# Kernel optimization log

Measured on AMD Instinct MI355X. Metric: run time of the kernel, lower is better.

The kernel has to match this reference:

```python
import jax, jax.numpy as jnp
import numpy as np

N = 1024
DIM = 128
HEADS = 8
DK = DIM // HEADS
EDIM = 16
EPS = 1e-5
NEG = -10000.0


def _lin(k, din, dout):
    return jax.random.normal(k, (din, dout), jnp.float32) * (1.0 / np.sqrt(din))


def setup_inputs() -> dict:
    key = jax.random.key(0)
    ks = jax.random.split(key, 10)
    mask = jax.random.randint(ks[2], (N, N), 0, 2).astype(bool)
    mask = mask | jnp.eye(N, dtype=bool)  # self-loops always valid
    return {
        "x": jax.random.normal(ks[0], (N, DIM), jnp.float32),
        "edge_feat": jax.random.normal(ks[1], (N, N, EDIM), jnp.float32),
        "mask": mask,
        "Wq": _lin(ks[3], DIM, DIM), "bq": jnp.zeros((DIM,), jnp.float32),
        "Wk": _lin(ks[4], DIM, DIM), "bk": jnp.zeros((DIM,), jnp.float32),
        "Wv": _lin(ks[5], DIM, DIM), "bv": jnp.zeros((DIM,), jnp.float32),
        "Wae": _lin(ks[6], EDIM, HEADS), "bae": jnp.zeros((HEADS,), jnp.float32),
        "Wve": _lin(ks[7], EDIM, DIM), "bve": jnp.zeros((DIM,), jnp.float32),
        "Wo": _lin(ks[8], DIM, DIM), "bo": jnp.zeros((DIM,), jnp.float32),
        "gamma": jnp.ones((DIM,), jnp.float32),
        "beta": jnp.zeros((DIM,), jnp.float32),
    }


def reference(x, edge_feat, mask, Wq, bq, Wk, bk, Wv, bv, Wae, bae, Wve, bve, Wo, bo, gamma, beta):
    n, dim = x.shape
    heads = bae.shape[0]
    dk = dim // heads
    # pre-LayerNorm
    mu = jnp.mean(x, axis=-1, keepdims=True)
    var = jnp.mean(jnp.square(x - mu), axis=-1, keepdims=True)
    h = (x - mu) * jax.lax.rsqrt(var + EPS) * gamma + beta
    q = (h @ Wq + bq).reshape(n, heads, dk)
    k = (h @ Wk + bk).reshape(n, heads, dk)
    v = (h @ Wv + bv).reshape(n, heads, dk)
    # attention logits with per-edge additive bias: (n, m, heads)
    att = jnp.einsum('nhd,mhd->nmh', q, k) / np.sqrt(dk).astype(np.float32)
    att = att + edge_feat @ Wae + bae
    att = jnp.where(mask[..., None], att, NEG)
    alpha = jax.nn.softmax(att, axis=1)  # softmax over source nodes m
    # edge-conditioned values: msg_{nm} = v_m + U(e_{nm})
    edge_val = (edge_feat @ Wve + bve).reshape(n, n, heads, dk)
    out = jnp.einsum('nmh,mhd->nhd', alpha, v) + jnp.einsum('nmh,nmhd->nhd', alpha, edge_val)
    out = out.reshape(n, dim) @ Wo + bo
    return x + out
```

## Files before the change

### kernel.cpp

```cpp
#include <hip/hip_runtime.h>
#include <hip/hip_bf16.h>

#define NNODE 1024
#define DIM 128
#define HEADS 8
#define DK 16
#define EDIM 16
#define BN 8
#define MR 32
#define KV_ROW 160
#define H_STRIDE 20
#define EF_ROW 20
#define EF_NSTR 644
#define LOG2E 1.44269504f

__global__ __launch_bounds__(384)
void ln_qkv_kernel(const float* __restrict__ x,
                   const float* __restrict__ Wq, const float* __restrict__ bq,
                   const float* __restrict__ Wk, const float* __restrict__ bk,
                   const float* __restrict__ Wv, const float* __restrict__ bv,
                   const float* __restrict__ gamma, const float* __restrict__ beta,
                   float* __restrict__ qg, float* __restrict__ kg, float* __restrict__ vg) {
    const int n = blockIdx.x;
    const int t = threadIdx.x;
    __shared__ float hrow[DIM];
    __shared__ float part[4];

    float xv = 0.f;
    if (t < 128) {
        xv = x[n * DIM + t];
        float v = xv;
        #pragma unroll
        for (int off = 32; off >= 1; off >>= 1) v += __shfl_xor(v, off);
        if ((t & 63) == 0) part[t >> 6] = v;
    }
    __syncthreads();
    const float mu = (part[0] + part[1]) * (1.0f / DIM);
    const float dx = xv - mu;
    if (t < 128) {
        float v = dx * dx;
        #pragma unroll
        for (int off = 32; off >= 1; off >>= 1) v += __shfl_xor(v, off);
        if ((t & 63) == 0) part[2 + (t >> 6)] = v;
    }
    __syncthreads();
    if (t < 128) {
        const float var = (part[2] + part[3]) * (1.0f / DIM);
        hrow[t] = dx * rsqrtf(var + 1e-5f) * gamma[t] + beta[t];
    }
    __syncthreads();

    const int which = t >> 7;
    const int col = t & 127;
    const float* W = (which == 0) ? Wq : (which == 1) ? Wk : Wv;
    const float* b = (which == 0) ? bq : (which == 1) ? bk : bv;
    float* o       = (which == 0) ? qg : (which == 1) ? kg : vg;
    float acc = b[col];
    #pragma unroll 16
    for (int i = 0; i < DIM; ++i) acc = fmaf(hrow[i], W[i * DIM + col], acc);
    o[n * DIM + col] = acc;
}

__global__ __launch_bounds__(256, 2)
void attn_kernel(const float* __restrict__ qg, const float* __restrict__ kg,
                 const float* __restrict__ vg, const float* __restrict__ ef,
                 const int* __restrict__ mask,
                 const float* __restrict__ Wae, const float* __restrict__ bae,
                 float* __restrict__ acc) {
    const int t = threadIdx.x;
    const int s  = t >> 5;
    const int np = (t >> 3) & 3;
    const int h  = t & 7;
    const int wid = t >> 6, lane = t & 63;
    const int bx = blockIdx.x;
    const int n0 = (bx >> 5) * BN;
    const int mb = (bx & 31) * MR;

    __shared__ float ef_lds[BN * EF_NSTR];
    __shared__ float kv_buf[2 * MR * KV_ROW];
    __shared__ int   mk_lds[BN * 34];

    float* k_lds = kv_buf;
    float* v_lds = kv_buf + MR * KV_ROW;

    #pragma unroll
    for (int r = 0; r < 4; ++r) {
        const int idx = t + 256 * r;
        const int nn = idx >> 7;
        const int mm = (idx >> 2) & 31;
        const int q4 = idx & 3;
        const float4 ev = *(const float4*)(ef + ((size_t)(n0 + nn) * NNODE + mb + mm) * EDIM + q4 * 4);
        *(float4*)&ef_lds[nn * EF_NSTR + mm * EF_ROW + q4 * 4] = ev;
    }
    #pragma unroll
    for (int r = 0; r < 4; ++r) {
        const int idx = t + 256 * r;
        const int mm = idx >> 5, c4 = idx & 31;
        const int hh = c4 >> 2, d4 = c4 & 3;
        const float4 kq = *(const float4*)(kg + (size_t)(mb + mm) * DIM + c4 * 4);
        const float4 vq = *(const float4*)(vg + (size_t)(mb + mm) * DIM + c4 * 4);
        *(float4*)&k_lds[mm * KV_ROW + hh * H_STRIDE + d4 * 4] = kq;
        *(float4*)&v_lds[mm * KV_ROW + hh * H_STRIDE + d4 * 4] = vq;
    }
    {
        const int nn = t >> 5, mm = t & 31;
        mk_lds[nn * 34 + mm] = mask[(size_t)(n0 + nn) * NNODE + (mb + mm)];
    }
    float qreg[2][DK];
    #pragma unroll
    for (int hf = 0; hf < 2; ++hf) {
        const float* qp = qg + (size_t)(n0 + np + 4 * hf) * DIM + h * DK;
        #pragma unroll
        for (int d4 = 0; d4 < 4; ++d4) {
            const float4 qv = *(const float4*)(qp + d4 * 4);
            qreg[hf][d4 * 4 + 0] = qv.x; qreg[hf][d4 * 4 + 1] = qv.y;
            qreg[hf][d4 * 4 + 2] = qv.z; qreg[hf][d4 * 4 + 3] = qv.w;
        }
    }
    float waec[EDIM];
    #pragma unroll
    for (int e = 0; e < EDIM; ++e) waec[e] = Wae[e * HEADS + h] * LOG2E;
    const float baeh = bae[h] * LOG2E;

    float sl[2] = {0.f, 0.f};
    float accv[2][DK], accT[2][EDIM];
    #pragma unroll
    for (int hf = 0; hf < 2; ++hf) {
        #pragma unroll
        for (int d = 0; d < DK; ++d) accv[hf][d] = 0.f;
        #pragma unroll
        for (int e = 0; e < EDIM; ++e) accT[hf][e] = 0.f;
    }

    __syncthreads();

    #pragma unroll
    for (int j = 0; j < 4; ++j) {
        const int m = j * 8 + s;
        float kk[DK], vv[DK];
        const float* kp = &k_lds[m * KV_ROW + h * H_STRIDE];
        const float* vp = &v_lds[m * KV_ROW + h * H_STRIDE];
        #pragma unroll
        for (int d4 = 0; d4 < 4; ++d4) {
            const float4 k4 = *(const float4*)(kp + d4 * 4);
            kk[d4 * 4 + 0] = k4.x; kk[d4 * 4 + 1] = k4.y;
            kk[d4 * 4 + 2] = k4.z; kk[d4 * 4 + 3] = k4.w;
            const float4 v4 = *(const float4*)(vp + d4 * 4);
            vv[d4 * 4 + 0] = v4.x; vv[d4 * 4 + 1] = v4.y;
            vv[d4 * 4 + 2] = v4.z; vv[d4 * 4 + 3] = v4.w;
        }
        #pragma unroll
        for (int hf = 0; hf < 2; ++hf) {
            const int n = np + 4 * hf;
            const float* ep = &ef_lds[n * EF_NSTR + m * EF_ROW];
            float efv[EDIM];
            #pragma unroll
            for (int e4 = 0; e4 < 4; ++e4) {
                const float4 ev = *(const float4*)(ep + e4 * 4);
                efv[e4 * 4 + 0] = ev.x; efv[e4 * 4 + 1] = ev.y;
                efv[e4 * 4 + 2] = ev.z; efv[e4 * 4 + 3] = ev.w;
            }
            float bias = baeh, dot = 0.f;
            #pragma unroll
            for (int e = 0; e < EDIM; ++e) bias = fmaf(efv[e], waec[e], bias);
            #pragma unroll
            for (int d = 0; d < DK; ++d) dot = fmaf(qreg[hf][d], kk[d], dot);
            const float lg = fmaf(dot, 0.25f * LOG2E, bias);
            const float p = mk_lds[n * 34 + m] ? __builtin_amdgcn_exp2f(lg) : 0.f;
            sl[hf] += p;
            #pragma unroll
            for (int d = 0; d < DK; ++d) accv[hf][d] = fmaf(p, vv[d], accv[hf][d]);
            #pragma unroll
            for (int e = 0; e < EDIM; ++e) accT[hf][e] = fmaf(p, efv[e], accT[hf][e]);
        }
    }

    #pragma unroll
    for (int hf = 0; hf < 2; ++hf) {
        sl[hf] += __shfl_xor(sl[hf], 32);
        #pragma unroll
        for (int d = 0; d < DK; ++d) accv[hf][d] += __shfl_xor(accv[hf][d], 32);
        #pragma unroll
        for (int e = 0; e < EDIM; ++e) accT[hf][e] += __shfl_xor(accT[hf][e], 32);
    }
    __syncthreads();
    float* red = kv_buf;
    if (lane < 32) {
        float* rp = &red[((wid * 4 + np) * 8 + h) * 66];
        #pragma unroll
        for (int hf = 0; hf < 2; ++hf) {
            rp[hf * 33 + 0] = sl[hf];
            #pragma unroll
            for (int d = 0; d < DK; ++d) rp[hf * 33 + 1 + d] = accv[hf][d];
            #pragma unroll
            for (int e = 0; e < EDIM; ++e) rp[hf * 33 + 17 + e] = accT[hf][e];
        }
    }
    __syncthreads();
    for (int v = t; v < BN * HEADS * 33; v += 256) {
        const int n = v / 264;
        const int rem = v - n * 264;
        const int hh = rem / 33;
        const int idx = rem - hh * 33;
        const int nnp = n & 3, hf = n >> 2;
        float sum = 0.f;
        #pragma unroll
        for (int w = 0; w < 4; ++w)
            sum += red[((w * 4 + nnp) * 8 + hh) * 66 + hf * 33 + idx];
        atomicAdd(&acc[((size_t)(n0 + n) * HEADS + hh) * 33 + idx], sum);
    }
}

__global__ __launch_bounds__(128)
void final_kernel(const float* __restrict__ acc,
                  const float* __restrict__ Wve, const float* __restrict__ bve,
                  const float* __restrict__ x,
                  const float* __restrict__ Wo, const float* __restrict__ bo,
                  float* __restrict__ out) {
    const int n = blockIdx.x, t = threadIdx.x;
    __shared__ float ab[HEADS * 33];
    __shared__ float orow[DIM];
    for (int u = t; u < HEADS * 33; u += 128) ab[u] = acc[(size_t)n * HEADS * 33 + u];
    __syncthreads();
    const int col = t, hh = col >> 4, dd = col & 15;
    const float slv = ab[hh * 33];
    float acc2 = 0.f;
    #pragma unroll
    for (int e = 0; e < EDIM; ++e) acc2 = fmaf(ab[hh * 33 + 17 + e], Wve[e * DIM + col], acc2);
    orow[col] = (ab[hh * 33 + 1 + dd] + acc2) / slv + bve[col];
    __syncthreads();
    float o = bo[col] + x[(size_t)n * DIM + col];
    #pragma unroll 16
    for (int i = 0; i < DIM; ++i) o = fmaf(orow[i], Wo[i * DIM + col], o);
    out[(size_t)n * DIM + col] = o;
}

extern "C" void kernel_launch(void* const* d_in, const int* in_sizes, int n_in,
                              void* d_out, int out_size, void* d_ws, size_t ws_size,
                              hipStream_t stream) {
    const float* x     = (const float*)d_in[0];
    const float* ef    = (const float*)d_in[1];
    const int*   mask  = (const int*)d_in[2];
    const float* Wq    = (const float*)d_in[3];
    const float* bq    = (const float*)d_in[4];
    const float* Wk    = (const float*)d_in[5];
    const float* bk    = (const float*)d_in[6];
    const float* Wv    = (const float*)d_in[7];
    const float* bv    = (const float*)d_in[8];
    const float* Wae   = (const float*)d_in[9];
    const float* bae   = (const float*)d_in[10];
    const float* Wve   = (const float*)d_in[11];
    const float* bve   = (const float*)d_in[12];
    const float* Wo    = (const float*)d_in[13];
    const float* bo    = (const float*)d_in[14];
    const float* gamma = (const float*)d_in[15];
    const float* beta  = (const float*)d_in[16];

    float* ws = (float*)d_ws;
    float* accb = ws;
    float* qg   = ws + 270336;
    float* kg   = qg + (size_t)NNODE * DIM;
    float* vg   = kg + (size_t)NNODE * DIM;

    hipMemsetAsync(accb, 0, (size_t)NNODE * HEADS * 33 * sizeof(float), stream);
    ln_qkv_kernel<<<NNODE, 384, 0, stream>>>(x, Wq, bq, Wk, bk, Wv, bv, gamma, beta, qg, kg, vg);
    attn_kernel<<<(NNODE / BN) * 32, 256, 0, stream>>>(qg, kg, vg, ef, mask, Wae, bae, accb);
    final_kernel<<<NNODE, 128, 0, stream>>>(accb, Wve, bve, x, Wo, bo, (float*)d_out);
}
```

Before: 183.3 us.

## Stage attention tiles in two smaller LDS chunks to raise occupancy

The attention kernel now loads the 32-source tile in two 16-source chunks, which shrinks LDS for edge features, K/V and mask. The launch bound moves from 2 to 4 blocks per SM. The cross-wave reduction becomes LDS atomics into a zeroed buffer in place of the write-then-sum pass, followed by a flat global atomic add. This trades one extra barrier and serialized per-chunk loads, plus LDS atomic contention, for higher occupancy and less shared memory.

```diff
diff --git a/kernel.cpp b/kernel.cpp
--- a/kernel.cpp
+++ b/kernel.cpp
@@ -8,10 +8,11 @@
 #define EDIM 16
 #define BN 8
 #define MR 32
+#define MC 16
 #define KV_ROW 160
 #define H_STRIDE 20
 #define EF_ROW 20
-#define EF_NSTR 644
+#define EF_NSTR 324
 #define LOG2E 1.44269504f
 
 __global__ __launch_bounds__(384)
@@ -61,7 +62,7 @@
     o[n * DIM + col] = acc;
 }
 
-__global__ __launch_bounds__(256, 2)
+__global__ __launch_bounds__(256, 4)
 void attn_kernel(const float* __restrict__ qg, const float* __restrict__ kg,
                  const float* __restrict__ vg, const float* __restrict__ ef,
                  const int* __restrict__ mask,
@@ -71,41 +72,19 @@
     const int s  = t >> 5;
     const int np = (t >> 3) & 3;
     const int h  = t & 7;
-    const int wid = t >> 6, lane = t & 63;
+    const int lane = t & 63;
     const int bx = blockIdx.x;
     const int n0 = (bx >> 5) * BN;
     const int mb = (bx & 31) * MR;
 
     __shared__ float ef_lds[BN * EF_NSTR];
-    __shared__ float kv_buf[2 * MR * KV_ROW];
-    __shared__ int   mk_lds[BN * 34];
-
-    float* k_lds = kv_buf;
-    float* v_lds = kv_buf + MR * KV_ROW;
-
-    #pragma unroll
-    for (int r = 0; r < 4; ++r) {
-        const int idx = t + 256 * r;
-        const int nn = idx >> 7;
-        const int mm = (idx >> 2) & 31;
-        const int q4 = idx & 3;
-        const float4 ev = *(const float4*)(ef + ((size_t)(n0 + nn) * NNODE + mb + mm) * EDIM + q4 * 4);
-        *(float4*)&ef_lds[nn * EF_NSTR + mm * EF_ROW + q4 * 4] = ev;
-    }
-    #pragma unroll
-    for (int r = 0; r < 4; ++r) {
-        const int idx = t + 256 * r;
-        const int mm = idx >> 5, c4 = idx & 31;
-        const int hh = c4 >> 2, d4 = c4 & 3;
-        const float4 kq = *(const float4*)(kg + (size_t)(mb + mm) * DIM + c4 * 4);
-        const float4 vq = *(const float4*)(vg + (size_t)(mb + mm) * DIM + c4 * 4);
-        *(float4*)&k_lds[mm * KV_ROW + hh * H_STRIDE + d4 * 4] = kq;
-        *(float4*)&v_lds[mm * KV_ROW + hh * H_STRIDE + d4 * 4] = vq;
-    }
-    {
-        const int nn = t >> 5, mm = t & 31;
-        mk_lds[nn * 34 + mm] = mask[(size_t)(n0 + nn) * NNODE + (mb + mm)];
-    }
+    __shared__ float k_lds[MC * KV_ROW];
+    __shared__ float v_lds[MC * KV_ROW];
+    __shared__ float red[BN * HEADS * 33];
+    __shared__ int   mk_lds[BN * 18];
+
+    for (int u = t; u < BN * HEADS * 33; u += 256) red[u] = 0.f;
+
     float qreg[2][DK];
     #pragma unroll
     for (int hf = 0; hf < 2; ++hf) {
@@ -132,46 +111,75 @@
         for (int e = 0; e < EDIM; ++e) accT[hf][e] = 0.f;
     }
 
-    __syncthreads();
-
-    #pragma unroll
-    for (int j = 0; j < 4; ++j) {
-        const int m = j * 8 + s;
-        float kk[DK], vv[DK];
-        const float* kp = &k_lds[m * KV_ROW + h * H_STRIDE];
-        const float* vp = &v_lds[m * KV_ROW + h * H_STRIDE];
-        #pragma unroll
-        for (int d4 = 0; d4 < 4; ++d4) {
-            const float4 k4 = *(const float4*)(kp + d4 * 4);
-            kk[d4 * 4 + 0] = k4.x; kk[d4 * 4 + 1] = k4.y;
-            kk[d4 * 4 + 2] = k4.z; kk[d4 * 4 + 3] = k4.w;
-            const float4 v4 = *(const float4*)(vp + d4 * 4);
-            vv[d4 * 4 + 0] = v4.x; vv[d4 * 4 + 1] = v4.y;
-            vv[d4 * 4 + 2] = v4.z; vv[d4 * 4 + 3] = v4.w;
-        }
-        #pragma unroll
-        for (int hf = 0; hf < 2; ++hf) {
-            const int n = np + 4 * hf;
-            const float* ep = &ef_lds[n * EF_NSTR + m * EF_ROW];
-            float efv[EDIM];
-            #pragma unroll
-            for (int e4 = 0; e4 < 4; ++e4) {
-                const float4 ev = *(const float4*)(ep + e4 * 4);
-                efv[e4 * 4 + 0] = ev.x; efv[e4 * 4 + 1] = ev.y;
-                efv[e4 * 4 + 2] = ev.z; efv[e4 * 4 + 3] = ev.w;
+    #pragma unroll
+    for (int c = 0; c < 2; ++c) {
+        const int mcb = mb + c * MC;
+        if (c) __syncthreads();
+
+        #pragma unroll
+        for (int r = 0; r < 2; ++r) {
+            const int idx = t + 256 * r;
+            const int nn = idx >> 6;
+            const int mm = (idx >> 2) & 15;
+            const int q4 = idx & 3;
+            const float4 ev = *(const float4*)(ef + ((size_t)(n0 + nn) * NNODE + mcb + mm) * EDIM + q4 * 4);
+            *(float4*)&ef_lds[nn * EF_NSTR + mm * EF_ROW + q4 * 4] = ev;
+        }
+        #pragma unroll
+        for (int r = 0; r < 2; ++r) {
+            const int idx = t + 256 * r;
+            const int mm = idx >> 5, c4 = idx & 31;
+            const int hh = c4 >> 2, d4 = c4 & 3;
+            const float4 kq = *(const float4*)(kg + (size_t)(mcb + mm) * DIM + c4 * 4);
+            const float4 vq = *(const float4*)(vg + (size_t)(mcb + mm) * DIM + c4 * 4);
+            *(float4*)&k_lds[mm * KV_ROW + hh * H_STRIDE + d4 * 4] = kq;
+            *(float4*)&v_lds[mm * KV_ROW + hh * H_STRIDE + d4 * 4] = vq;
+        }
+        if (t < BN * MC) {
+            const int nn = t >> 4, mm = t & 15;
+            mk_lds[nn * 18 + mm] = mask[(size_t)(n0 + nn) * NNODE + mcb + mm];
+        }
+        __syncthreads();
+
+        #pragma unroll
+        for (int j = 0; j < 2; ++j) {
+            const int m = j * 8 + s;
+            float kk[DK], vv[DK];
+            const float* kp = &k_lds[m * KV_ROW + h * H_STRIDE];
+            const float* vp = &v_lds[m * KV_ROW + h * H_STRIDE];
+            #pragma unroll
+            for (int d4 = 0; d4 < 4; ++d4) {
+                const float4 k4 = *(const float4*)(kp + d4 * 4);
+                kk[d4 * 4 + 0] = k4.x; kk[d4 * 4 + 1] = k4.y;
+                kk[d4 * 4 + 2] = k4.z; kk[d4 * 4 + 3] = k4.w;
+                const float4 v4 = *(const float4*)(vp + d4 * 4);
+                vv[d4 * 4 + 0] = v4.x; vv[d4 * 4 + 1] = v4.y;
+                vv[d4 * 4 + 2] = v4.z; vv[d4 * 4 + 3] = v4.w;
             }
-            float bias = baeh, dot = 0.f;
-            #pragma unroll
-            for (int e = 0; e < EDIM; ++e) bias = fmaf(efv[e], waec[e], bias);
-            #pragma unroll
-            for (int d = 0; d < DK; ++d) dot = fmaf(qreg[hf][d], kk[d], dot);
-            const float lg = fmaf(dot, 0.25f * LOG2E, bias);
-            const float p = mk_lds[n * 34 + m] ? __builtin_amdgcn_exp2f(lg) : 0.f;
-            sl[hf] += p;
-            #pragma unroll
-            for (int d = 0; d < DK; ++d) accv[hf][d] = fmaf(p, vv[d], accv[hf][d]);
-            #pragma unroll
-            for (int e = 0; e < EDIM; ++e) accT[hf][e] = fmaf(p, efv[e], accT[hf][e]);
+            #pragma unroll
+            for (int hf = 0; hf < 2; ++hf) {
+                const int n = np + 4 * hf;
+                const float* ep = &ef_lds[n * EF_NSTR + m * EF_ROW];
+                float efv[EDIM];
+                #pragma unroll
+                for (int e4 = 0; e4 < 4; ++e4) {
+                    const float4 ev = *(const float4*)(ep + e4 * 4);
+                    efv[e4 * 4 + 0] = ev.x; efv[e4 * 4 + 1] = ev.y;
+                    efv[e4 * 4 + 2] = ev.z; efv[e4 * 4 + 3] = ev.w;
+                }
+                float bias = baeh, dot = 0.f;
+                #pragma unroll
+                for (int e = 0; e < EDIM; ++e) bias = fmaf(efv[e], waec[e], bias);
+                #pragma unroll
+                for (int d = 0; d < DK; ++d) dot = fmaf(qreg[hf][d], kk[d], dot);
+                const float lg = fmaf(dot, 0.25f * LOG2E, bias);
+                const float p = mk_lds[n * 18 + m] ? __builtin_amdgcn_exp2f(lg) : 0.f;
+                sl[hf] += p;
+                #pragma unroll
+                for (int d = 0; d < DK; ++d) accv[hf][d] = fmaf(p, vv[d], accv[hf][d]);
+                #pragma unroll
+                for (int e = 0; e < EDIM; ++e) accT[hf][e] = fmaf(p, efv[e], accT[hf][e]);
+            }
         }
     }
 
@@ -183,32 +191,20 @@
         #pragma unroll
         for (int e = 0; e < EDIM; ++e) accT[hf][e] += __shfl_xor(accT[hf][e], 32);
     }
-    __syncthreads();
-    float* red = kv_buf;
     if (lane < 32) {
-        float* rp = &red[((wid * 4 + np) * 8 + h) * 66];
         #pragma unroll
         for (int hf = 0; hf < 2; ++hf) {
-            rp[hf * 33 + 0] = sl[hf];
-            #pragma unroll
-            for (int d = 0; d < DK; ++d) rp[hf * 33 + 1 + d] = accv[hf][d];
-            #pragma unroll
-            for (int e = 0; e < EDIM; ++e) rp[hf * 33 + 17 + e] = accT[hf][e];
-        }
-    }
-    __syncthreads();
-    for (int v = t; v < BN * HEADS * 33; v += 256) {
-        const int n = v / 264;
-        const int rem = v - n * 264;
-        const int hh = rem / 33;
-        const int idx = rem - hh * 33;
-        const int nnp = n & 3, hf = n >> 2;
-        float sum = 0.f;
-        #pragma unroll
-        for (int w = 0; w < 4; ++w)
-            sum += red[((w * 4 + nnp) * 8 + hh) * 66 + hf * 33 + idx];
-        atomicAdd(&acc[((size_t)(n0 + n) * HEADS + hh) * 33 + idx], sum);
-    }
+            float* rp = &red[((np + 4 * hf) * 8 + h) * 33];
+            atomicAdd(&rp[0], sl[hf]);
+            #pragma unroll
+            for (int d = 0; d < DK; ++d) atomicAdd(&rp[1 + d], accv[hf][d]);
+            #pragma unroll
+            for (int e = 0; e < EDIM; ++e) atomicAdd(&rp[17 + e], accT[hf][e]);
+        }
+    }
+    __syncthreads();
+    for (int u = t; u < BN * HEADS * 33; u += 256)
+        atomicAdd(&acc[(size_t)n0 * HEADS * 33 + u], red[u]);
 }
 
 __global__ __launch_bounds__(128)
```

Result: slower. 527.6 us (+187.8%).

## Read K/V directly from global memory and reuse edge-feature LDS for reduction

Applied to the files above, without the earlier changes.

Drops the shared-memory staging of K and V tiles. The attention loop now loads them straight from global memory through the cache, and that loop is no longer unrolled. The cross-wave reduction is rebuilt to reuse the edge-feature LDS buffer as two partial-sum arrays, with waves 2–3 accumulating into the values written by waves 0–1. The aim is to cut LDS footprint (raising occupancy) and staging overhead, at the cost of more global/L2 loads per thread, less instruction-level parallelism from the un-unrolled loop, and an extra barrier stage.

```diff
diff --git a/kernel.cpp b/kernel.cpp
--- a/kernel.cpp
+++ b/kernel.cpp
@@ -8,8 +8,6 @@
 #define EDIM 16
 #define BN 8
 #define MR 32
-#define KV_ROW 160
-#define H_STRIDE 20
 #define EF_ROW 20
 #define EF_NSTR 644
 #define LOG2E 1.44269504f
@@ -77,11 +75,7 @@
     const int mb = (bx & 31) * MR;
 
     __shared__ float ef_lds[BN * EF_NSTR];
-    __shared__ float kv_buf[2 * MR * KV_ROW];
     __shared__ int   mk_lds[BN * 34];
-
-    float* k_lds = kv_buf;
-    float* v_lds = kv_buf + MR * KV_ROW;
 
     #pragma unroll
     for (int r = 0; r < 4; ++r) {
@@ -92,16 +86,6 @@
         const float4 ev = *(const float4*)(ef + ((size_t)(n0 + nn) * NNODE + mb + mm) * EDIM + q4 * 4);
         *(float4*)&ef_lds[nn * EF_NSTR + mm * EF_ROW + q4 * 4] = ev;
     }
-    #pragma unroll
-    for (int r = 0; r < 4; ++r) {
-        const int idx = t + 256 * r;
-        const int mm = idx >> 5, c4 = idx & 31;
-        const int hh = c4 >> 2, d4 = c4 & 3;
-        const float4 kq = *(const float4*)(kg + (size_t)(mb + mm) * DIM + c4 * 4);
-        const float4 vq = *(const float4*)(vg + (size_t)(mb + mm) * DIM + c4 * 4);
-        *(float4*)&k_lds[mm * KV_ROW + hh * H_STRIDE + d4 * 4] = kq;
-        *(float4*)&v_lds[mm * KV_ROW + hh * H_STRIDE + d4 * 4] = vq;
-    }
     {
         const int nn = t >> 5, mm = t & 31;
         mk_lds[nn * 34 + mm] = mask[(size_t)(n0 + nn) * NNODE + (mb + mm)];
@@ -134,12 +118,13 @@
 
     __syncthreads();
 
-    #pragma unroll
+    #pragma unroll 1
     for (int j = 0; j < 4; ++j) {
         const int m = j * 8 + s;
+        const size_t gm = (size_t)(mb + m);
         float kk[DK], vv[DK];
-        const float* kp = &k_lds[m * KV_ROW + h * H_STRIDE];
-        const float* vp = &v_lds[m * KV_ROW + h * H_STRIDE];
+        const float* kp = kg + gm * DIM + h * DK;
+        const float* vp = vg + gm * DIM + h * DK;
         #pragma unroll
         for (int d4 = 0; d4 < 4; ++d4) {
             const float4 k4 = *(const float4*)(kp + d4 * 4);
@@ -184,31 +169,36 @@
         for (int e = 0; e < EDIM; ++e) accT[hf][e] += __shfl_xor(accT[hf][e], 32);
     }
     __syncthreads();
-    float* red = kv_buf;
-    if (lane < 32) {
-        float* rp = &red[((wid * 4 + np) * 8 + h) * 66];
+    float* redA = ef_lds;
+    float* redB = ef_lds + BN * HEADS * 33;
+    if (lane < 32 && wid < 2) {
+        float* base = (wid == 0) ? redA : redB;
         #pragma unroll
         for (int hf = 0; hf < 2; ++hf) {
-            rp[hf * 33 + 0] = sl[hf];
-            #pragma unroll
-            for (int d = 0; d < DK; ++d) rp[hf * 33 + 1 + d] = accv[hf][d];
-            #pragma unroll
-            for (int e = 0; e < EDIM; ++e) rp[hf * 33 + 17 + e] = accT[hf][e];
-        }
-    }
-    __syncthreads();
-    for (int v = t; v < BN * HEADS * 33; v += 256) {
-        const int n = v / 264;
-        const int rem = v - n * 264;
-        const int hh = rem / 33;
-        const int idx = rem - hh * 33;
-        const int nnp = n & 3, hf = n >> 2;
-        float sum = 0.f;
-        #pragma unroll
-        for (int w = 0; w < 4; ++w)
-            sum += red[((w * 4 + nnp) * 8 + hh) * 66 + hf * 33 + idx];
-        atomicAdd(&acc[((size_t)(n0 + n) * HEADS + hh) * 33 + idx], sum);
-    }
+            float* rp = base + ((np + 4 * hf) * 8 + h) * 33;
+            rp[0] = sl[hf];
+            #pragma unroll
+            for (int d = 0; d < DK; ++d) rp[1 + d] = accv[hf][d];
+            #pragma unroll
+            for (int e = 0; e < EDIM; ++e) rp[17 + e] = accT[hf][e];
+        }
+    }
+    __syncthreads();
+    if (lane < 32 && wid >= 2) {
+        float* base = (wid == 2) ? redA : redB;
+        #pragma unroll
+        for (int hf = 0; hf < 2; ++hf) {
+            float* rp = base + ((np + 4 * hf) * 8 + h) * 33;
+            rp[0] += sl[hf];
+            #pragma unroll
+            for (int d = 0; d < DK; ++d) rp[1 + d] += accv[hf][d];
+            #pragma unroll
+            for (int e = 0; e < EDIM; ++e) rp[17 + e] += accT[hf][e];
+        }
+    }
+    __syncthreads();
+    for (int u = t; u < BN * HEADS * 33; u += 256)
+        atomicAdd(&acc[(size_t)n0 * HEADS * 33 + u], redA[u] + redB[u]);
 }
 
 __global__ __launch_bounds__(128)
```

Result: slower. 200.4 us (+9.3%).
